# Kernel tuning notes

Measured on AMD Instinct MI355X. Metric: run time of the kernel, lower is better.

## Reference

```python
import jax, jax.numpy as jnp
import numpy as np
from jax.ops import segment_sum

N_NODES = 50000
N_EDGES = 800000
IN_FEATS = 128
H_FEATS = 256
NUM_CLASSES = 16


def setup_inputs() -> dict:
    key = jax.random.key(0)
    k1, k2, k3, k4, k5 = jax.random.split(key, 5)
    in_feat = jax.random.normal(k1, (N_NODES, IN_FEATS), dtype=jnp.float32)
    src = jax.random.randint(k2, (N_EDGES,), 0, N_NODES, dtype=jnp.int32)
    dst = jax.random.randint(k3, (N_EDGES,), 0, N_NODES, dtype=jnp.int32)
    # Glorot-ish scaled params
    W_gc = jax.random.normal(k4, (IN_FEATS, H_FEATS), dtype=jnp.float32) / np.sqrt(IN_FEATS)
    b_gc = jnp.zeros((H_FEATS,), dtype=jnp.float32)
    W_fc = jax.random.normal(k5, (H_FEATS, NUM_CLASSES), dtype=jnp.float32) / np.sqrt(H_FEATS)
    b_fc = jnp.zeros((NUM_CLASSES,), dtype=jnp.float32)
    return {"in_feat": in_feat, "src": src, "dst": dst,
            "W_gc": W_gc, "b_gc": b_gc, "W_fc": W_fc, "b_fc": b_fc}


def reference(in_feat, src, dst, W_gc, b_gc, W_fc, b_fc):
    n = in_feat.shape[0]
    ones = jnp.ones_like(src, dtype=in_feat.dtype)
    # DGL GraphConv, norm='both': D_out^{-1/2} on source side, sum-aggregate,
    # D_in^{-1/2} on destination side. Degrees clamped to >= 1.
    deg_out = jnp.clip(segment_sum(ones, src, num_segments=n), 1.0)
    deg_in = jnp.clip(segment_sum(ones, dst, num_segments=n), 1.0)
    x = in_feat * jax.lax.rsqrt(deg_out)[:, None]            # [N, in]
    agg = segment_sum(x[src], dst, num_segments=n)           # [N, in] irregular gather+scatter
    agg = agg * jax.lax.rsqrt(deg_in)[:, None]
    # in_feats <= h_feats -> aggregate first, then project (DGL ordering)
    h = agg @ W_gc + b_gc                                    # [N, h]
    h = jax.nn.relu(h)
    logits = h @ W_fc + b_fc                                 # [N, num_classes]
    return jax.nn.sigmoid(logits)
```

## Files before the change

### kernel.cpp

```cpp
#include <hip/hip_runtime.h>
#include <hip/hip_bf16.h>

#define IN_F  128
#define H_F   256
#define NC    16
#define BM    64
#define CAP   64
#define PCAP  8192

typedef short bf16x8 __attribute__((ext_vector_type(8)));
typedef float f32x4  __attribute__((ext_vector_type(4)));

__device__ __forceinline__ unsigned short f2bf(float x) {
    union { float f; unsigned u; } v; v.f = x;
    unsigned r = v.u + 0x7FFF + ((v.u >> 16) & 1);
    return (unsigned short)(r >> 16);
}
__device__ __forceinline__ float bf2f(unsigned h) {
    union { unsigned u; float f; } v; v.u = h << 16; return v.f;
}

__global__ void gcn_zero(int* __restrict__ cur) {
    int tid = threadIdx.x;
    cur[tid] = 0;
    cur[tid + 256] = 0;
}

__global__ __launch_bounds__(256) void gcn_part(
    const int* __restrict__ src, const int* __restrict__ dst,
    int* __restrict__ curS, int* __restrict__ curD,
    unsigned short* __restrict__ srcP, unsigned* __restrict__ dstP,
    const float* __restrict__ W_gc, const float* __restrict__ W_fc,
    unsigned short* __restrict__ Wp, unsigned short* __restrict__ Wfp,
    const float* __restrict__ in_feat, unsigned* __restrict__ xb,
    int n_edges, int n_feat4, int nb_edge, int np) {
    __shared__ int cS[256], cD[256];
    int b0 = blockIdx.x, tid = threadIdx.x;
    if (b0 < nb_edge) {
        unsigned sv[16], dv[16];
        int ebase = b0 * 4096;
        #pragma unroll
        for (int r = 0; r < 16; ++r) {
            int e = ebase + r * 256 + tid;
            if (e < n_edges) { sv[r] = (unsigned)src[e]; dv[r] = (unsigned)dst[e]; }
            else { sv[r] = 0xFFFFFFFFu; dv[r] = 0xFFFFFFFFu; }
        }
        cS[tid] = 0; cD[tid] = 0;
        __syncthreads();
        #pragma unroll
        for (int r = 0; r < 16; ++r) {
            if (dv[r] != 0xFFFFFFFFu) {
                atomicAdd(&cS[sv[r] >> 8], 1);
                atomicAdd(&cD[dv[r] >> 8], 1);
            }
        }
        __syncthreads();
        if (tid < np) {
            int c = cS[tid];
            cS[tid] = c ? atomicAdd(&curS[tid], c) : 0;
            c = cD[tid];
            cD[tid] = c ? atomicAdd(&curD[tid], c) : 0;
        }
        __syncthreads();
        #pragma unroll
        for (int r = 0; r < 16; ++r) {
            if (dv[r] != 0xFFFFFFFFu) {
                unsigned s = sv[r], d = dv[r];
                int ps = atomicAdd(&cS[s >> 8], 1);
                if (ps < PCAP) srcP[(size_t)(s >> 8) * PCAP + ps] = (unsigned short)s;
                int pd = atomicAdd(&cD[d >> 8], 1);
                if (pd < PCAP) dstP[(size_t)(d >> 8) * PCAP + pd] =
                    ((d & 255u) << 16) | (s & 0xffffu);
            }
        }
        return;
    }
    int b = b0 - nb_edge;
    if (b < 128) {
        int g = b * 256 + tid;
        {
            int j = g & 7, l = (g >> 3) & 63, t = g >> 9;
            int kt = t & 3, ct = t >> 2;
            int k = kt * 32 + ((l >> 4) << 3) + j;
            int col = ct * 16 + (l & 15);
            Wp[g] = f2bf(W_gc[k * 256 + col]);
        }
        if (g < 4096) {
            int j = g & 7, l = (g >> 3) & 63, kt = g >> 9;
            int k = kt * 32 + ((l >> 4) << 3) + j;
            Wfp[g] = f2bf(W_fc[k * 16 + (l & 15)]);
        }
        return;
    }
    int idx = (b - 128) * 256 + tid;
    if (idx < n_feat4) {
        float4 v = ((const float4*)in_feat)[idx];
        uint2 o;
        o.x = (unsigned)f2bf(v.x) | ((unsigned)f2bf(v.y) << 16);
        o.y = (unsigned)f2bf(v.z) | ((unsigned)f2bf(v.w) << 16);
        ((uint2*)xb)[idx] = o;
    }
}

__global__ __launch_bounds__(256) void gcn_bucket(
    const unsigned short* __restrict__ srcP, const unsigned* __restrict__ dstP,
    const int* __restrict__ curS, const int* __restrict__ curD,
    int* __restrict__ cnt_out, int* __restrict__ cnt_in,
    unsigned short* __restrict__ esrc, int n, int np) {
    __shared__ unsigned hist[256];
    __shared__ unsigned short bucket[256 * CAP];
    int p = blockIdx.x, tid = threadIdx.x;
    hist[tid] = 0;
    __syncthreads();
    if (p < np) {
        int cnt = curS[p]; if (cnt > PCAP) cnt = PCAP;
        const unsigned short* sp = srcP + (size_t)p * PCAP;
        for (int i = tid; i < cnt; i += 256)
            atomicAdd(&hist[sp[i] & 255], 1);
        __syncthreads();
        int node = p * 256 + tid;
        if (node < n) cnt_out[node] = (int)hist[tid];
    } else {
        int pp = p - np;
        int cnt = curD[pp]; if (cnt > PCAP) cnt = PCAP;
        const unsigned* dp = dstP + (size_t)pp * PCAP;
        for (int i = tid; i < cnt; i += 256) {
            unsigned pair = dp[i];
            unsigned dl = pair >> 16;
            unsigned pos = atomicAdd(&hist[dl], 1);
            if (pos < CAP) bucket[(dl << 6) + pos] = (unsigned short)(pair & 0xffffu);
        }
        __syncthreads();
        unsigned* eb = (unsigned*)(esrc + ((size_t)pp << 14));
        const unsigned* bu = (const unsigned*)bucket;
        int maxrow = n - pp * 256;
        int words = (maxrow >= 256) ? 8192 : (maxrow > 0 ? maxrow * 32 : 0);
        for (int i = tid; i < words; i += 256) eb[i] = bu[i];
        int node = pp * 256 + tid;
        if (node < n) cnt_in[node] = (int)hist[tid];
    }
}

__global__ __launch_bounds__(256) void gcn_aggregate(
    const unsigned* __restrict__ xb, const unsigned short* __restrict__ esrc,
    const int* __restrict__ cnt_in, const int* __restrict__ cnt_out,
    unsigned* __restrict__ aggb, int n) {
    int wave = (blockIdx.x * blockDim.x + threadIdx.x) >> 6;
    int lane = threadIdx.x & 63;
    if (wave >= n) return;
    int wv = __builtin_amdgcn_readfirstlane(wave);
    int cnt = cnt_in[wv];
    if (cnt > CAP) cnt = CAP;
    const unsigned short* es = esrc + ((size_t)wv << 6);
    float ax[8], ay[8];
    #pragma unroll
    for (int u = 0; u < 8; ++u) { ax[u] = 0.f; ay[u] = 0.f; }
    for (int i = 0; i < cnt; i += 16) {
        uint4 pa = *(const uint4*)(es + i);
        uint4 pb = *(const uint4*)(es + i + 8);
        unsigned wrd[8];
        wrd[0] = pa.x; wrd[1] = pa.y; wrd[2] = pa.z; wrd[3] = pa.w;
        wrd[4] = pb.x; wrd[5] = pb.y; wrd[6] = pb.z; wrd[7] = pb.w;
        int rem = cnt - i;
        int sidx[16];
        float rs[16];
        #pragma unroll
        for (int k = 0; k < 16; ++k) {
            int s = (int)((wrd[k >> 1] >> ((k & 1) * 16)) & 0xffffu);
            sidx[k] = (k < rem) ? s : 0;
        }
        #pragma unroll
        for (int k = 0; k < 16; ++k)
            rs[k] = (k < rem) ? rsqrtf((float)cnt_out[sidx[k]]) : 0.f;
        unsigned vv[16];
        #pragma unroll
        for (int k = 0; k < 16; ++k)
            vv[k] = xb[(size_t)sidx[k] * 64 + lane];
        #pragma unroll
        for (int k = 0; k < 16; ++k) {
            ax[k & 7] = fmaf(bf2f(vv[k] & 0xffffu), rs[k], ax[k & 7]);
            ay[k & 7] = fmaf(bf2f(vv[k] >> 16),     rs[k], ay[k & 7]);
        }
    }
    float axs = ((ax[0] + ax[1]) + (ax[2] + ax[3])) + ((ax[4] + ax[5]) + (ax[6] + ax[7]));
    float ays = ((ay[0] + ay[1]) + (ay[2] + ay[3])) + ((ay[4] + ay[5]) + (ay[6] + ay[7]));
    float ri = rsqrtf(fmaxf((float)cnt, 1.0f));
    aggb[(size_t)wave * 64 + lane] =
        (unsigned)f2bf(axs * ri) | ((unsigned)f2bf(ays * ri) << 16);
}

__global__ __launch_bounds__(256) void gcn_mlp(
    const unsigned* __restrict__ aggb, const unsigned short* __restrict__ Wp,
    const unsigned short* __restrict__ Wfp, const float* __restrict__ b_gc,
    const float* __restrict__ b_fc, float* __restrict__ out, int n) {
    extern __shared__ char smraw[];
    unsigned short* Wl  = (unsigned short*)smraw;
    unsigned short* Wfl = Wl + 32768;
    unsigned short* Al  = Wfl + 4096;
    unsigned short* Hl  = Al + 8192;
    float* bgl = (float*)(Hl + 16384);
    float* bfl = bgl + 256;

    int tid = threadIdx.x;
    int lane = tid & 63, w = tid >> 6;

    for (int i = tid; i < 4096; i += 256) ((float4*)Wl)[i]  = ((const float4*)Wp)[i];
    for (int i = tid; i < 512;  i += 256) ((float4*)Wfl)[i] = ((const float4*)Wfp)[i];
    bgl[tid] = b_gc[tid];
    if (tid < NC) bfl[tid] = b_fc[tid];

    int ntiles = (n + BM - 1) / BM;
    for (int tile = blockIdx.x; tile < ntiles; tile += gridDim.x) {
        __syncthreads();
        int row0 = tile * BM;
        for (int i = tid; i < 1024; i += 256) {
            int r = i >> 4, cb = i & 15;
            int node = row0 + r;
            float4 v = (node < n) ? ((const float4*)aggb)[(size_t)node * 16 + cb]
                                  : make_float4(0.f, 0.f, 0.f, 0.f);
            ((float4*)Al)[r * 16 + (cb ^ (r & 7))] = v;
        }
        __syncthreads();

        bf16x8 af[4];
        {
            int r = lane & 15;
            #pragma unroll
            for (int kt = 0; kt < 4; ++kt) {
                int cb = kt * 4 + (lane >> 4);
                af[kt] = *((const bf16x8*)Al + ((w * 16 + r) * 16 + (cb ^ (r & 7))));
            }
        }
        f32x4 acc[16];
        #pragma unroll
        for (int ct = 0; ct < 16; ++ct) {
            acc[ct] = (f32x4){0.f, 0.f, 0.f, 0.f};
            #pragma unroll
            for (int kt = 0; kt < 4; ++kt) {
                bf16x8 bfr = *((const bf16x8*)Wl + ((ct * 4 + kt) * 64 + lane));
                acc[ct] = __builtin_amdgcn_mfma_f32_16x16x32_bf16(af[kt], bfr, acc[ct], 0, 0, 0);
            }
        }
        #pragma unroll
        for (int ct = 0; ct < 16; ++ct) {
            int col = ct * 16 + (lane & 15);
            float bv = bgl[col];
            #pragma unroll
            for (int r4 = 0; r4 < 4; ++r4) {
                int r = ((lane >> 4) << 2) + r4;
                float hv = fmaxf(acc[ct][r4] + bv, 0.f);
                int cu = col >> 3;
                Hl[(w * 16 + r) * 256 + ((cu ^ (r & 7)) << 3) + (col & 7)] = f2bf(hv);
            }
        }
        f32x4 acc2 = (f32x4){0.f, 0.f, 0.f, 0.f};
        {
            int r = lane & 15;
            #pragma unroll
            for (int kt = 0; kt < 8; ++kt) {
                int cu = kt * 4 + (lane >> 4);
                bf16x8 a2 = *((const bf16x8*)Hl + ((w * 16 + r) * 32 + (cu ^ (r & 7))));
                bf16x8 b2 = *((const bf16x8*)Wfl + (kt * 64 + lane));
                acc2 = __builtin_amdgcn_mfma_f32_16x16x32_bf16(a2, b2, acc2, 0, 0, 0);
            }
        }
        int col = lane & 15;
        float bv = bfl[col];
        #pragma unroll
        for (int r4 = 0; r4 < 4; ++r4) {
            int row = row0 + w * 16 + ((lane >> 4) << 2) + r4;
            if (row < n) {
                float v = acc2[r4] + bv;
                out[(size_t)row * NC + col] = 1.f / (1.f + expf(-v));
            }
        }
    }
}

extern "C" void kernel_launch(void* const* d_in, const int* in_sizes, int n_in,
                              void* d_out, int out_size, void* d_ws, size_t ws_size,
                              hipStream_t stream) {
    const float* in_feat = (const float*)d_in[0];
    const int*   src     = (const int*)d_in[1];
    const int*   dst     = (const int*)d_in[2];
    const float* W_gc    = (const float*)d_in[3];
    const float* b_gc    = (const float*)d_in[4];
    const float* W_fc    = (const float*)d_in[5];
    const float* b_fc    = (const float*)d_in[6];
    float* out = (float*)d_out;

    int n_nodes = in_sizes[0] / IN_F;
    int n_edges = in_sizes[1];
    int np = (n_nodes + 255) >> 8;

    int* curS = (int*)d_ws;
    int* curD = curS + 256;
    int* cnt_out = curD + 256;
    int* cnt_in  = cnt_out + n_nodes;
    unsigned short* srcP = (unsigned short*)(cnt_in + n_nodes);
    unsigned* dstP = (unsigned*)(srcP + (size_t)np * PCAP);
    unsigned short* esrc = (unsigned short*)(dstP + (size_t)np * PCAP);
    unsigned short* Wp   = esrc + (size_t)np * 256 * CAP;
    unsigned short* Wfp  = Wp + 32768;
    unsigned* xb   = (unsigned*)(Wfp + 4096);
    unsigned* aggb = xb + (size_t)n_nodes * 64;

    gcn_zero<<<1, 256, 0, stream>>>(curS);

    {
        int n_feat4 = n_nodes * 32;
        int nb_edge = (n_edges + 4095) / 4096;
        int nb_conv = (n_feat4 + 255) / 256;
        gcn_part<<<nb_edge + 128 + nb_conv, 256, 0, stream>>>(
            src, dst, curS, curD, srcP, dstP, W_gc, W_fc, Wp, Wfp,
            in_feat, xb, n_edges, n_feat4, nb_edge, np);
    }
    gcn_bucket<<<2 * np, 256, 0, stream>>>(srcP, dstP, curS, curD,
                                           cnt_out, cnt_in, esrc, n_nodes, np);
    {
        int blocks = (n_nodes + 3) / 4;
        gcn_aggregate<<<blocks, 256, 0, stream>>>(xb, esrc, cnt_in, cnt_out, aggb, n_nodes);
    }
    {
        size_t smem = 65536 + 8192 + 16384 + 32768 + 1024 + 64;
        hipFuncSetAttribute((const void*)gcn_mlp,
                            hipFuncAttributeMaxDynamicSharedMemorySize, (int)smem);
        gcn_mlp<<<256, 256, smem, stream>>>(aggb, Wp, Wfp, b_gc, b_fc, out, n_nodes);
    }
}
```

Before: 103.0 us.

## Prescale bf16 features by out-degree norm and gather two edges per wave

The source-side D_out^{-1/2} scaling now happens once per node inside the bucket kernel, which rewrites the bf16 feature table in place. This removes the per-edge cnt_out lookup and rsqrt from aggregation. Bucket slots are padded with a dummy node index pointing at a zero row appended to xb, so the aggregate loop needs no bounds masking. Each wave splits into two halves that gather different edges with 8-byte loads and combine the halves with a cross-lane shuffle. The cost is an extra read-modify-write pass over the feature table and an additional rounding to bf16 after scaling.

```diff
diff --git a/kernel.cpp b/kernel.cpp
--- a/kernel.cpp
+++ b/kernel.cpp
@@ -16,14 +16,18 @@
     unsigned r = v.u + 0x7FFF + ((v.u >> 16) & 1);
     return (unsigned short)(r >> 16);
 }
-__device__ __forceinline__ float bf2f(unsigned h) {
-    union { unsigned u; float f; } v; v.u = h << 16; return v.f;
-}
-
-__global__ void gcn_zero(int* __restrict__ cur) {
+__device__ __forceinline__ float bflo(unsigned x) {
+    union { unsigned u; float f; } v; v.u = x << 16; return v.f;
+}
+__device__ __forceinline__ float bfhi(unsigned x) {
+    union { unsigned u; float f; } v; v.u = x & 0xffff0000u; return v.f;
+}
+
+__global__ void gcn_zero(int* __restrict__ cur, unsigned* __restrict__ xb, int n) {
     int tid = threadIdx.x;
     cur[tid] = 0;
     cur[tid + 256] = 0;
+    if (tid < 64) xb[(size_t)n * 64 + tid] = 0;
 }
 
 __global__ __launch_bounds__(256) void gcn_part(
@@ -106,8 +110,10 @@
     const unsigned short* __restrict__ srcP, const unsigned* __restrict__ dstP,
     const int* __restrict__ curS, const int* __restrict__ curD,
     int* __restrict__ cnt_out, int* __restrict__ cnt_in,
-    unsigned short* __restrict__ esrc, int n, int np) {
+    unsigned short* __restrict__ esrc, unsigned* __restrict__ xb,
+    int n, int np) {
     __shared__ unsigned hist[256];
+    __shared__ float rr[256];
     __shared__ unsigned short bucket[256 * CAP];
     int p = blockIdx.x, tid = threadIdx.x;
     hist[tid] = 0;
@@ -120,10 +126,27 @@
         __syncthreads();
         int node = p * 256 + tid;
         if (node < n) cnt_out[node] = (int)hist[tid];
+        rr[tid] = rsqrtf(fmaxf((float)hist[tid], 1.0f));
+        __syncthreads();
+        for (int i = tid; i < 16384; i += 256) {
+            int row = i >> 6, el = i & 63;
+            int nd = p * 256 + row;
+            if (nd < n) {
+                unsigned v = xb[(size_t)nd * 64 + el];
+                float r = rr[row];
+                float lo = bflo(v) * r;
+                float hi = bfhi(v) * r;
+                xb[(size_t)nd * 64 + el] = (unsigned)f2bf(lo) | ((unsigned)f2bf(hi) << 16);
+            }
+        }
     } else {
         int pp = p - np;
+        unsigned dummy2 = ((unsigned)n & 0xffffu) | (((unsigned)n & 0xffffu) << 16);
+        unsigned* bu32 = (unsigned*)bucket;
+        for (int i = tid; i < 8192; i += 256) bu32[i] = dummy2;
         int cnt = curD[pp]; if (cnt > PCAP) cnt = PCAP;
         const unsigned* dp = dstP + (size_t)pp * PCAP;
+        __syncthreads();
         for (int i = tid; i < cnt; i += 256) {
             unsigned pair = dp[i];
             unsigned dl = pair >> 16;
@@ -143,8 +166,7 @@
 
 __global__ __launch_bounds__(256) void gcn_aggregate(
     const unsigned* __restrict__ xb, const unsigned short* __restrict__ esrc,
-    const int* __restrict__ cnt_in, const int* __restrict__ cnt_out,
-    unsigned* __restrict__ aggb, int n) {
+    const int* __restrict__ cnt_in, unsigned* __restrict__ aggb, int n) {
     int wave = (blockIdx.x * blockDim.x + threadIdx.x) >> 6;
     int lane = threadIdx.x & 63;
     if (wave >= n) return;
@@ -152,41 +174,42 @@
     int cnt = cnt_in[wv];
     if (cnt > CAP) cnt = CAP;
     const unsigned short* es = esrc + ((size_t)wv << 6);
-    float ax[8], ay[8];
+    const uint2* xb2 = (const uint2*)xb;
+    int half = lane >> 5;
+    int sub  = lane & 31;
+    int hsh  = half * 16;
+    float a0[8], a1[8], a2[8], a3[8];
     #pragma unroll
-    for (int u = 0; u < 8; ++u) { ax[u] = 0.f; ay[u] = 0.f; }
+    for (int j = 0; j < 8; ++j) { a0[j] = 0.f; a1[j] = 0.f; a2[j] = 0.f; a3[j] = 0.f; }
     for (int i = 0; i < cnt; i += 16) {
         uint4 pa = *(const uint4*)(es + i);
         uint4 pb = *(const uint4*)(es + i + 8);
         unsigned wrd[8];
         wrd[0] = pa.x; wrd[1] = pa.y; wrd[2] = pa.z; wrd[3] = pa.w;
         wrd[4] = pb.x; wrd[5] = pb.y; wrd[6] = pb.z; wrd[7] = pb.w;
-        int rem = cnt - i;
-        int sidx[16];
-        float rs[16];
-        #pragma unroll
-        for (int k = 0; k < 16; ++k) {
-            int s = (int)((wrd[k >> 1] >> ((k & 1) * 16)) & 0xffffu);
-            sidx[k] = (k < rem) ? s : 0;
-        }
-        #pragma unroll
-        for (int k = 0; k < 16; ++k)
-            rs[k] = (k < rem) ? rsqrtf((float)cnt_out[sidx[k]]) : 0.f;
-        unsigned vv[16];
-        #pragma unroll
-        for (int k = 0; k < 16; ++k)
-            vv[k] = xb[(size_t)sidx[k] * 64 + lane];
-        #pragma unroll
-        for (int k = 0; k < 16; ++k) {
-            ax[k & 7] = fmaf(bf2f(vv[k] & 0xffffu), rs[k], ax[k & 7]);
-            ay[k & 7] = fmaf(bf2f(vv[k] >> 16),     rs[k], ay[k & 7]);
-        }
-    }
-    float axs = ((ax[0] + ax[1]) + (ax[2] + ax[3])) + ((ax[4] + ax[5]) + (ax[6] + ax[7]));
-    float ays = ((ay[0] + ay[1]) + (ay[2] + ay[3])) + ((ay[4] + ay[5]) + (ay[6] + ay[7]));
-    float ri = rsqrtf(fmaxf((float)cnt, 1.0f));
-    aggb[(size_t)wave * 64 + lane] =
-        (unsigned)f2bf(axs * ri) | ((unsigned)f2bf(ays * ri) << 16);
+        #pragma unroll
+        for (int j = 0; j < 8; ++j) {
+            int s = (int)((wrd[j] >> hsh) & 0xffffu);
+            uint2 v = xb2[(size_t)s * 32 + sub];
+            a0[j] += bflo(v.x); a1[j] += bfhi(v.x);
+            a2[j] += bflo(v.y); a3[j] += bfhi(v.y);
+        }
+    }
+    float s0 = ((a0[0]+a0[1])+(a0[2]+a0[3]))+((a0[4]+a0[5])+(a0[6]+a0[7]));
+    float s1 = ((a1[0]+a1[1])+(a1[2]+a1[3]))+((a1[4]+a1[5])+(a1[6]+a1[7]));
+    float s2 = ((a2[0]+a2[1])+(a2[2]+a2[3]))+((a2[4]+a2[5])+(a2[6]+a2[7]));
+    float s3 = ((a3[0]+a3[1])+(a3[2]+a3[3]))+((a3[4]+a3[5])+(a3[6]+a3[7]));
+    s0 += __shfl_xor(s0, 32);
+    s1 += __shfl_xor(s1, 32);
+    s2 += __shfl_xor(s2, 32);
+    s3 += __shfl_xor(s3, 32);
+    if (half == 0) {
+        float ri = rsqrtf(fmaxf((float)cnt, 1.0f));
+        uint2 o;
+        o.x = (unsigned)f2bf(s0 * ri) | ((unsigned)f2bf(s1 * ri) << 16);
+        o.y = (unsigned)f2bf(s2 * ri) | ((unsigned)f2bf(s3 * ri) << 16);
+        ((uint2*)aggb)[(size_t)wv * 32 + sub] = o;
+    }
 }
 
 __global__ __launch_bounds__(256) void gcn_mlp(
@@ -303,9 +326,9 @@
     unsigned short* Wp   = esrc + (size_t)np * 256 * CAP;
     unsigned short* Wfp  = Wp + 32768;
     unsigned* xb   = (unsigned*)(Wfp + 4096);
-    unsigned* aggb = xb + (size_t)n_nodes * 64;
-
-    gcn_zero<<<1, 256, 0, stream>>>(curS);
+    unsigned* aggb = xb + (size_t)(n_nodes + 1) * 64;
+
+    gcn_zero<<<1, 256, 0, stream>>>(curS, xb, n_nodes);
 
     {
         int n_feat4 = n_nodes * 32;
@@ -316,10 +339,10 @@
             in_feat, xb, n_edges, n_feat4, nb_edge, np);
     }
     gcn_bucket<<<2 * np, 256, 0, stream>>>(srcP, dstP, curS, curD,
-                                           cnt_out, cnt_in, esrc, n_nodes, np);
+                                           cnt_out, cnt_in, esrc, xb, n_nodes, np);
     {
         int blocks = (n_nodes + 3) / 4;
-        gcn_aggregate<<<blocks, 256, 0, stream>>>(xb, esrc, cnt_in, cnt_out, aggb, n_nodes);
+        gcn_aggregate<<<blocks, 256, 0, stream>>>(xb, esrc, cnt_in, aggb, n_nodes);
     }
     {
         size_t smem = 65536 + 8192 + 16384 + 32768 + 1024 + 64;
```

After: 104.9 us. No clear change (+1.8%).
